# Kernel tuning notes

Measured on AMD Instinct MI355X. Metric: run time of the kernel, lower is better.

The kernel has to match this reference:

```python
import jax, jax.numpy as jnp
import numpy as np

N = 50000   # nodes
E = 800000  # edges (avg degree 16)
IN, H, OUT = 128, 128, 64


def setup_inputs() -> dict:
    key = jax.random.key(0)
    ks = jax.random.split(key, 8)

    def w(k, shape):
        fan_in = shape[0]
        return (jax.random.normal(k, shape, jnp.float32) / np.float32(np.sqrt(fan_in)))

    x = jax.random.normal(ks[0], (N, IN), jnp.float32)
    edge_index = jax.random.randint(ks[1], (2, E), 0, N, jnp.int64)
    return {
        "x": x,
        "edge_index": edge_index,
        "W1": w(ks[2], (IN, H)), "b1": jnp.zeros((H,), jnp.float32),
        "W2": w(ks[3], (H, H)),  "b2": jnp.zeros((H,), jnp.float32),
        "W3": w(ks[4], (H, H)),  "b3": jnp.zeros((H,), jnp.float32),
        "Wd1": w(ks[5], (H, H)), "bd1": jnp.zeros((H,), jnp.float32),
        "Wd2": w(ks[6], (H, OUT)), "bd2": jnp.zeros((OUT,), jnp.float32),
    }


def _gcn_conv(x, src, dst, norm, W, b):
    # x: [N, Cin] -> linear transform, gather along edges, normalized scatter-add
    h = x @ W                                   # [N, Cout]
    msg = h[src] * norm[:, None]                # [E+N, Cout]
    out = jax.ops.segment_sum(msg, dst, num_segments=N)
    return out + b


def reference(x, edge_index, W1, b1, W2, b2, W3, b3, Wd1, bd1, Wd2, bd2):
    # Add self-loops (PyG GCNConv default) and compute symmetric normalization.
    loops = jnp.arange(N, dtype=edge_index.dtype)
    src = jnp.concatenate([edge_index[0], loops])   # [E+N]
    dst = jnp.concatenate([edge_index[1], loops])   # [E+N]
    deg = jax.ops.segment_sum(jnp.ones_like(dst, dtype=x.dtype), dst, num_segments=N)
    dinv = jnp.where(deg > 0, jax.lax.rsqrt(deg), jnp.zeros_like(deg))
    norm = dinv[src] * dinv[dst]                    # [E+N]

    h = jax.nn.relu(_gcn_conv(x, src, dst, norm, W1, b1))
    h = jax.nn.relu(_gcn_conv(h, src, dst, norm, W2, b2))
    h = jax.nn.relu(_gcn_conv(h, src, dst, norm, W3, b3))

    h = jax.nn.relu(h @ Wd1 + bd1)
    return jax.nn.sigmoid(h @ Wd2 + bd2)            # [N, OUT]
```

## Files before the change

kernel.cpp:

```cpp
#include <hip/hip_runtime.h>
#include <hip/hip_bf16.h>
#include <hip/hip_fp16.h>

#define N_NODES 50000
#define N_EDGES 800000
#define C_H 128
#define C_OUT 64
#define NBLK 196
#define TSTRIDE 136
#define E_PAD 950272
#define MM_BLKS 782

typedef __attribute__((ext_vector_type(8))) short bf16x8;
typedef __attribute__((ext_vector_type(4))) float f32x4;

static __device__ __forceinline__ float bf_lo(unsigned int u) { return __uint_as_float(u << 16); }
static __device__ __forceinline__ float bf_hi(unsigned int u) { return __uint_as_float(u & 0xffff0000u); }
static __device__ __forceinline__ unsigned short f2bf(float f) {
    __hip_bfloat16 h = __float2bfloat16(f);
    return *(unsigned short*)&h;
}
static __device__ __forceinline__ unsigned int pack2(float a, float b) {
    return (unsigned int)f2bf(a) | ((unsigned int)f2bf(b) << 16);
}
static __device__ __forceinline__ unsigned short f2h_bits(float f) {
    union { __half h; unsigned short u; } c; c.h = __float2half_rn(f); return c.u;
}
static __device__ __forceinline__ float h_bits2f(unsigned short u) {
    union { __half h; unsigned short u; } c; c.u = u; return __half2float(c.h);
}

__global__ void prep_kernel(const int* __restrict__ dst, int* __restrict__ counts,
                            int* __restrict__ rank,
                            const float* __restrict__ W1, const float* __restrict__ W2,
                            const float* __restrict__ W3, const float* __restrict__ Wd1,
                            const float* __restrict__ Wd2,
                            unsigned short* __restrict__ P1, unsigned short* __restrict__ P2,
                            unsigned short* __restrict__ P3, unsigned short* __restrict__ Pd1,
                            unsigned short* __restrict__ Pd2,
                            unsigned int* __restrict__ epay) {
    int b = blockIdx.x;
    if (b < 3125) {
        int e = b * 256 + threadIdx.x;
        rank[e] = atomicAdd(&counts[dst[e]], 1);
    } else if (b < 3413) {
        int idx = (b - 3125) * 256 + threadIdx.x;
        if (idx < 4 * 16384) {
            int which = idx >> 14;
            int r = idx & 16383;
            const float* W = (which == 0) ? W1 : (which == 1) ? W2 : (which == 2) ? W3 : Wd1;
            unsigned short* P = (which == 0) ? P1 : (which == 1) ? P2 : (which == 2) ? P3 : Pd1;
            int j = r & 7, lane = (r >> 3) & 63, t = r >> 9;
            int nb = t & 7, kb = t >> 3;
            int k = kb * 32 + ((lane >> 4) << 3) + j;
            int n = nb * 16 + (lane & 15);
            P[r] = f2bf(W[(size_t)k * 128 + n]);
        } else {
            int r = idx - 65536;
            if (r < 8192) {
                int j = r & 7, lane = (r >> 3) & 63, t = r >> 9;
                int nb = t & 3, kb = t >> 2;
                int k = kb * 32 + ((lane >> 4) << 3) + j;
                int n = nb * 16 + (lane & 15);
                Pd2[r] = f2bf(Wd2[(size_t)k * 64 + n]);
            }
        }
    } else {
        int i = (b - 3413) * 256 + threadIdx.x;
        *(uint4*)(epay + (size_t)i * 4) = make_uint4(0, 0, 0, 0);
    }
}

__global__ void __launch_bounds__(256) scan1_kernel(const int* __restrict__ counts,
                                                    int* __restrict__ eblk,
                                                    int* __restrict__ bsum,
                                                    float* __restrict__ dinv) {
    __shared__ int ws[4];
    int i = blockIdx.x * 256 + threadIdx.x;
    int v = (i < N_NODES) ? counts[i] : 0;
    if (i < N_NODES) dinv[i] = rsqrtf((float)v + 1.0f);
    int vp = (v + 3) & ~3;
    int lane = threadIdx.x & 63, w = threadIdx.x >> 6;
    int x = vp;
    #pragma unroll
    for (int off = 1; off < 64; off <<= 1) {
        int t = __shfl_up(x, off, 64);
        if (lane >= off) x += t;
    }
    if (lane == 63) ws[w] = x;
    __syncthreads();
    if (threadIdx.x == 0) {
        int run = 0;
        #pragma unroll
        for (int k = 0; k < 4; ++k) { int t = ws[k]; ws[k] = run; run += t; }
        bsum[blockIdx.x] = run;
    }
    __syncthreads();
    if (i < N_NODES) eblk[i] = x - vp + ws[w];
}

__global__ void __launch_bounds__(256) scan2_kernel(const int* __restrict__ bsum,
                                                    int* __restrict__ bo,
                                                    int* __restrict__ rowptr) {
    __shared__ int ws[4];
    int i = threadIdx.x;
    int v = (i < NBLK) ? bsum[i] : 0;
    int lane = i & 63, w = i >> 6;
    int x = v;
    #pragma unroll
    for (int off = 1; off < 64; off <<= 1) {
        int t = __shfl_up(x, off, 64);
        if (lane >= off) x += t;
    }
    if (lane == 63) ws[w] = x;
    __syncthreads();
    if (i == 0) {
        int run = 0;
        #pragma unroll
        for (int k = 0; k < 4; ++k) { int t = ws[k]; ws[k] = run; run += t; }
    }
    __syncthreads();
    int excl = x - v + ws[w];
    if (i < NBLK) bo[i] = excl;
    if (i == 255) rowptr[N_NODES] = excl + v;
}

__global__ void scan3_kernel(const int* __restrict__ eblk, const int* __restrict__ bo,
                             int* __restrict__ rowptr) {
    int i = blockIdx.x * 256 + threadIdx.x;
    if (i < N_NODES) rowptr[i] = eblk[i] + bo[blockIdx.x];
}

__global__ void __launch_bounds__(256) fill_mm_kernel(
        const float* __restrict__ x, const unsigned short* __restrict__ P1,
        unsigned short* __restrict__ XW1,
        const int* __restrict__ src, const int* __restrict__ dst,
        const float* __restrict__ dinv,
        const int* __restrict__ rowptr, const int* __restrict__ rank,
        unsigned int* __restrict__ epay) {
    int b = blockIdx.x;
    if (b < MM_BLKS) {
        const int lane = threadIdx.x & 63;
        const int wave = threadIdx.x >> 6;
        const int wid  = b * 4 + wave;
        if (wid * 16 >= N_NODES) return;
        const int node = wid * 16 + (lane & 15);
        const int quad = lane >> 4;
        f32x4 acc[8];
        #pragma unroll
        for (int nb = 0; nb < 8; ++nb) acc[nb] = (f32x4){0.f, 0.f, 0.f, 0.f};
        #pragma unroll
        for (int kb = 0; kb < 4; ++kb) {
            const float* p = x + (size_t)node * 128 + kb * 32 + quad * 8;
            float4 lo = *(const float4*)p;
            float4 hi = *(const float4*)(p + 4);
            union { bf16x8 v; unsigned int u[4]; } tmp;
            tmp.u[0] = pack2(lo.x, lo.y); tmp.u[1] = pack2(lo.z, lo.w);
            tmp.u[2] = pack2(hi.x, hi.y); tmp.u[3] = pack2(hi.z, hi.w);
            #pragma unroll
            for (int nb = 0; nb < 8; ++nb) {
                bf16x8 wf = *(const bf16x8*)(P1 + ((size_t)(kb * 8 + nb) * 64 + lane) * 8);
                acc[nb] = __builtin_amdgcn_mfma_f32_16x16x32_bf16(wf, tmp.v, acc[nb], 0, 0, 0);
            }
        }
        #pragma unroll
        for (int nb = 0; nb < 8; ++nb) {
            int ch = nb * 16 + quad * 4;
            uint2 o;
            o.x = pack2(acc[nb][0], acc[nb][1]);
            o.y = pack2(acc[nb][2], acc[nb][3]);
            *(uint2*)(XW1 + (size_t)node * C_H + ch) = o;
        }
    } else {
        int e = (b - MM_BLKS) * 256 + threadIdx.x;
        if (e < N_EDGES) {
            int d = dst[e], s = src[e];
            int pos = rowptr[d] + rank[e];
            float nrm = dinv[s] * dinv[d];
            epay[pos] = (unsigned int)s | ((unsigned int)f2h_bits(nrm) << 16);
        }
    }
}

struct Acc8 { float a0, a1, a2, a3, a4, a5, a6, a7; };

static __device__ __forceinline__ unsigned int ev_comp(const uint4 ea, const uint4 eb, int j) {
    switch (j) {
        case 0: return ea.x; case 1: return ea.y; case 2: return ea.z; case 3: return ea.w;
        case 4: return eb.x; case 5: return eb.y; case 6: return eb.z; default: return eb.w;
    }
}
static __device__ __forceinline__ unsigned int ev_comp4(const uint4 ev, int j) {
    switch (j) { case 0: return ev.x; case 1: return ev.y; case 2: return ev.z; default: return ev.w; }
}

#define ROW_FMA(rv, nm) \
    r.a0 = fmaf(bf_lo((rv).x), nm, r.a0); r.a1 = fmaf(bf_hi((rv).x), nm, r.a1); \
    r.a2 = fmaf(bf_lo((rv).y), nm, r.a2); r.a3 = fmaf(bf_hi((rv).y), nm, r.a3); \
    r.a4 = fmaf(bf_lo((rv).z), nm, r.a4); r.a5 = fmaf(bf_hi((rv).z), nm, r.a5); \
    r.a6 = fmaf(bf_lo((rv).w), nm, r.a6); r.a7 = fmaf(bf_hi((rv).w), nm, r.a7);

static __device__ __forceinline__ Acc8 agg_row(
        const int* __restrict__ rowptr,
        const unsigned int* __restrict__ epay,
        const unsigned short* __restrict__ hin,
        const float* __restrict__ dinv,
        int node, int c8) {
    const unsigned short* hc = hin + c8;
    float di = dinv[node], dii = di * di;
    uint4 raw = *(const uint4*)(hc + (size_t)node * C_H);
    Acc8 r;
    r.a0 = bf_lo(raw.x) * dii; r.a1 = bf_hi(raw.x) * dii;
    r.a2 = bf_lo(raw.y) * dii; r.a3 = bf_hi(raw.y) * dii;
    r.a4 = bf_lo(raw.z) * dii; r.a5 = bf_hi(raw.z) * dii;
    r.a6 = bf_lo(raw.w) * dii; r.a7 = bf_hi(raw.w) * dii;

    int beg = rowptr[node], end = rowptr[node + 1];
    int deg = end - beg;
    int n8 = deg >> 3;
    int tail = (deg >> 2) & 1;
    const unsigned int* ep = epay + beg;

    if (n8 > 0) {
        uint4 e0a = *(const uint4*)(ep);
        uint4 e0b = *(const uint4*)(ep + 4);
        uint4 r0[8];
        #pragma unroll
        for (int j = 0; j < 8; ++j)
            r0[j] = *(const uint4*)(hc + (size_t)(ev_comp(e0a, e0b, j) & 0xffffu) * C_H);
        uint4 e1a, e1b;
        if (n8 > 1) {
            e1a = *(const uint4*)(ep + 8);
            e1b = *(const uint4*)(ep + 12);
        }
        for (int k = 0; k + 2 < n8; ++k) {
            uint4 r1[8];
            #pragma unroll
            for (int j = 0; j < 8; ++j)
                r1[j] = *(const uint4*)(hc + (size_t)(ev_comp(e1a, e1b, j) & 0xffffu) * C_H);
            uint4 e2a = *(const uint4*)(ep + ((k + 2) << 3));
            uint4 e2b = *(const uint4*)(ep + ((k + 2) << 3) + 4);
            #pragma unroll
            for (int j = 0; j < 8; ++j) {
                float nm = h_bits2f((unsigned short)(ev_comp(e0a, e0b, j) >> 16));
                ROW_FMA(r0[j], nm);
            }
            e0a = e1a; e0b = e1b; e1a = e2a; e1b = e2b;
            #pragma unroll
            for (int j = 0; j < 8; ++j) r0[j] = r1[j];
        }
        if (n8 > 1) {
            uint4 r1[8];
            #pragma unroll
            for (int j = 0; j < 8; ++j)
                r1[j] = *(const uint4*)(hc + (size_t)(ev_comp(e1a, e1b, j) & 0xffffu) * C_H);
            #pragma unroll
            for (int j = 0; j < 8; ++j) {
                float nm = h_bits2f((unsigned short)(ev_comp(e0a, e0b, j) >> 16));
                ROW_FMA(r0[j], nm);
            }
            #pragma unroll
            for (int j = 0; j < 8; ++j) {
                float nm = h_bits2f((unsigned short)(ev_comp(e1a, e1b, j) >> 16));
                ROW_FMA(r1[j], nm);
            }
        } else {
            #pragma unroll
            for (int j = 0; j < 8; ++j) {
                float nm = h_bits2f((unsigned short)(ev_comp(e0a, e0b, j) >> 16));
                ROW_FMA(r0[j], nm);
            }
        }
    }
    if (tail) {
        uint4 ev = *(const uint4*)(ep + (n8 << 3));
        uint4 rv[4];
        #pragma unroll
        for (int j = 0; j < 4; ++j)
            rv[j] = *(const uint4*)(hc + (size_t)(ev_comp4(ev, j) & 0xffffu) * C_H);
        #pragma unroll
        for (int j = 0; j < 4; ++j) {
            float nm = h_bits2f((unsigned short)(ev_comp4(ev, j) >> 16));
            ROW_FMA(rv[j], nm);
        }
    }
    return r;
}

__global__ void __launch_bounds__(256) gather1_kernel(
        const int* __restrict__ rowptr,
        const unsigned int* __restrict__ epay,
        const float* __restrict__ dinv,
        const unsigned short* __restrict__ hin,
        const float* __restrict__ bias,
        unsigned short* __restrict__ out) {
    int t    = blockIdx.x * 256 + threadIdx.x;
    int node = t >> 4;
    int c8   = (t & 15) << 3;

    Acc8 r = agg_row(rowptr, epay, hin, dinv, node, c8);

    float4 ba = *(const float4*)(bias + c8);
    float4 bb = *(const float4*)(bias + c8 + 4);
    float a0 = fmaxf(r.a0 + ba.x, 0.f), a1 = fmaxf(r.a1 + ba.y, 0.f);
    float a2 = fmaxf(r.a2 + ba.z, 0.f), a3 = fmaxf(r.a3 + ba.w, 0.f);
    float a4 = fmaxf(r.a4 + bb.x, 0.f), a5 = fmaxf(r.a5 + bb.y, 0.f);
    float a6 = fmaxf(r.a6 + bb.z, 0.f), a7 = fmaxf(r.a7 + bb.w, 0.f);
    uint4 o;
    o.x = pack2(a0, a1); o.y = pack2(a2, a3);
    o.z = pack2(a4, a5); o.w = pack2(a6, a7);
    *(uint4*)(out + (size_t)node * C_H + c8) = o;
}

template <bool FINAL>
__global__ void __launch_bounds__(256) fused_layer_kernel(
        const int* __restrict__ rowptr,
        const unsigned int* __restrict__ epay,
        const float* __restrict__ dinv,
        const unsigned short* __restrict__ hin,
        const unsigned short* __restrict__ Wp,
        const float* __restrict__ bias,
        const unsigned short* __restrict__ Wd1p,
        const float* __restrict__ bd1,
        const unsigned short* __restrict__ Wd2p,
        const float* __restrict__ bd2,
        unsigned short* __restrict__ out_b,
        float* __restrict__ out_f) {
    __shared__ unsigned short sG[16 * TSTRIDE];
    const int t = threadIdx.x;

    {
        int nl = t >> 4, c8 = (t & 15) << 3;
        int node = blockIdx.x * 16 + nl;
        Acc8 r = agg_row(rowptr, epay, hin, dinv, node, c8);
        uint4 o;
        o.x = pack2(r.a0, r.a1); o.y = pack2(r.a2, r.a3);
        o.z = pack2(r.a4, r.a5); o.w = pack2(r.a6, r.a7);
        *(uint4*)(sG + nl * TSTRIDE + c8) = o;
    }
    __syncthreads();

    const int lane = t & 63, wave = t >> 6, quad = lane >> 4, row = lane & 15;
    const int node = blockIdx.x * 16 + row;

    f32x4 acc0 = (f32x4){0.f, 0.f, 0.f, 0.f};
    f32x4 acc1 = (f32x4){0.f, 0.f, 0.f, 0.f};
    const int nb0 = 2 * wave, nb1 = 2 * wave + 1;
    #pragma unroll
    for (int kb = 0; kb < 4; ++kb) {
        bf16x8 hf = *(const bf16x8*)(sG + row * TSTRIDE + kb * 32 + quad * 8);
        bf16x8 wf0 = *(const bf16x8*)(Wp + ((size_t)(kb * 8 + nb0) * 64 + lane) * 8);
        bf16x8 wf1 = *(const bf16x8*)(Wp + ((size_t)(kb * 8 + nb1) * 64 + lane) * 8);
        acc0 = __builtin_amdgcn_mfma_f32_16x16x32_bf16(wf0, hf, acc0, 0, 0, 0);
        acc1 = __builtin_amdgcn_mfma_f32_16x16x32_bf16(wf1, hf, acc1, 0, 0, 0);
    }
    float4 ba0 = *(const float4*)(bias + nb0 * 16 + quad * 4);
    float4 ba1 = *(const float4*)(bias + nb1 * 16 + quad * 4);
    float v00 = fmaxf(acc0[0] + ba0.x, 0.f), v01 = fmaxf(acc0[1] + ba0.y, 0.f);
    float v02 = fmaxf(acc0[2] + ba0.z, 0.f), v03 = fmaxf(acc0[3] + ba0.w, 0.f);
    float v10 = fmaxf(acc1[0] + ba1.x, 0.f), v11 = fmaxf(acc1[1] + ba1.y, 0.f);
    float v12 = fmaxf(acc1[2] + ba1.z, 0.f), v13 = fmaxf(acc1[3] + ba1.w, 0.f);

    if (!FINAL) {
        uint2 o0, o1;
        o0.x = pack2(v00, v01); o0.y = pack2(v02, v03);
        o1.x = pack2(v10, v11); o1.y = pack2(v12, v13);
        *(uint2*)(out_b + (size_t)node * C_H + nb0 * 16 + quad * 4) = o0;
        *(uint2*)(out_b + (size_t)node * C_H + nb1 * 16 + quad * 4) = o1;
        return;
    }

    __syncthreads();
    {
        uint2 o0, o1;
        o0.x = pack2(v00, v01); o0.y = pack2(v02, v03);
        o1.x = pack2(v10, v11); o1.y = pack2(v12, v13);
        *(uint2*)(sG + row * TSTRIDE + nb0 * 16 + quad * 4) = o0;
        *(uint2*)(sG + row * TSTRIDE + nb1 * 16 + quad * 4) = o1;
    }
    __syncthreads();

    acc0 = (f32x4){0.f, 0.f, 0.f, 0.f};
    acc1 = (f32x4){0.f, 0.f, 0.f, 0.f};
    #pragma unroll
    for (int kb = 0; kb < 4; ++kb) {
        bf16x8 hf = *(const bf16x8*)(sG + row * TSTRIDE + kb * 32 + quad * 8);
        bf16x8 wf0 = *(const bf16x8*)(Wd1p + ((size_t)(kb * 8 + nb0) * 64 + lane) * 8);
        bf16x8 wf1 = *(const bf16x8*)(Wd1p + ((size_t)(kb * 8 + nb1) * 64 + lane) * 8);
        acc0 = __builtin_amdgcn_mfma_f32_16x16x32_bf16(wf0, hf, acc0, 0, 0, 0);
        acc1 = __builtin_amdgcn_mfma_f32_16x16x32_bf16(wf1, hf, acc1, 0, 0, 0);
    }
    ba0 = *(const float4*)(bd1 + nb0 * 16 + quad * 4);
    ba1 = *(const float4*)(bd1 + nb1 * 16 + quad * 4);
    v00 = fmaxf(acc0[0] + ba0.x, 0.f); v01 = fmaxf(acc0[1] + ba0.y, 0.f);
    v02 = fmaxf(acc0[2] + ba0.z, 0.f); v03 = fmaxf(acc0[3] + ba0.w, 0.f);
    v10 = fmaxf(acc1[0] + ba1.x, 0.f); v11 = fmaxf(acc1[1] + ba1.y, 0.f);
    v12 = fmaxf(acc1[2] + ba1.z, 0.f); v13 = fmaxf(acc1[3] + ba1.w, 0.f);
    __syncthreads();
    {
        uint2 o0, o1;
        o0.x = pack2(v00, v01); o0.y = pack2(v02, v03);
        o1.x = pack2(v10, v11); o1.y = pack2(v12, v13);
        *(uint2*)(sG + row * TSTRIDE + nb0 * 16 + quad * 4) = o0;
        *(uint2*)(sG + row * TSTRIDE + nb1 * 16 + quad * 4) = o1;
    }
    __syncthreads();

    f32x4 acc = (f32x4){0.f, 0.f, 0.f, 0.f};
    #pragma unroll
    for (int kb = 0; kb < 4; ++kb) {
        bf16x8 hf = *(const bf16x8*)(sG + row * TSTRIDE + kb * 32 + quad * 8);
        bf16x8 wf = *(const bf16x8*)(Wd2p + ((size_t)(kb * 4 + wave) * 64 + lane) * 8);
        acc = __builtin_amdgcn_mfma_f32_16x16x32_bf16(wf, hf, acc, 0, 0, 0);
    }
    int ch = wave * 16 + quad * 4;
    float4 b4 = *(const float4*)(bd2 + ch);
    float4 rr;
    rr.x = 1.f / (1.f + expf(-(acc[0] + b4.x)));
    rr.y = 1.f / (1.f + expf(-(acc[1] + b4.y)));
    rr.z = 1.f / (1.f + expf(-(acc[2] + b4.z)));
    rr.w = 1.f / (1.f + expf(-(acc[3] + b4.w)));
    *(float4*)(out_f + (size_t)node * C_OUT + ch) = rr;
}

extern "C" void kernel_launch(void* const* d_in, const int* in_sizes, int n_in,
                              void* d_out, int out_size, void* d_ws, size_t ws_size,
                              hipStream_t stream) {
    const float* x   = (const float*)d_in[0];
    const int*   ei  = (const int*)d_in[1];
    const float* W1  = (const float*)d_in[2];
    const float* b1  = (const float*)d_in[3];
    const float* W2  = (const float*)d_in[4];
    const float* b2  = (const float*)d_in[5];
    const float* W3  = (const float*)d_in[6];
    const float* b3  = (const float*)d_in[7];
    const float* Wd1 = (const float*)d_in[8];
    const float* bd1 = (const float*)d_in[9];
    const float* Wd2 = (const float*)d_in[10];
    const float* bd2 = (const float*)d_in[11];

    const int* src = ei;
    const int* dst = ei + N_EDGES;

    char* base = (char*)d_ws;
    size_t off = 0;
    auto alloc = [&](size_t bytes) { char* p = base + off; off += (bytes + 255) & ~size_t(255); return p; };
    int*            counts = (int*)alloc(50176 * 4);
    unsigned int*   epay   = (unsigned int*)alloc((size_t)E_PAD * 4);
    int*            rank   = (int*)alloc((size_t)N_EDGES * 4);
    float*          dinv   = (float*)alloc(N_NODES * 4);
    int*            rowptr = (int*)alloc((N_NODES + 1) * 4);
    int*            eblk   = (int*)alloc(N_NODES * 4);
    int*            bsum   = (int*)alloc(256 * 4);
    int*            bo     = (int*)alloc(256 * 4);
    unsigned short* XW1    = (unsigned short*)alloc((size_t)N_NODES * C_H * 2);
    unsigned short* bufA   = (unsigned short*)alloc((size_t)N_NODES * C_H * 2);
    unsigned short* bufB   = (unsigned short*)alloc((size_t)N_NODES * C_H * 2);
    unsigned short* P1     = (unsigned short*)alloc(128 * 128 * 2);
    unsigned short* P2     = (unsigned short*)alloc(128 * 128 * 2);
    unsigned short* P3     = (unsigned short*)alloc(128 * 128 * 2);
    unsigned short* Pd1    = (unsigned short*)alloc(128 * 128 * 2);
    unsigned short* Pd2    = (unsigned short*)alloc(128 * 64 * 2);

    const int T = 256;
    dim3 blk(T);
    dim3 gN((N_NODES + T - 1) / T);
    dim3 gPrep(3125 + 288 + 928);
    dim3 gFillMM(MM_BLKS + 3125);
    dim3 gFused(N_NODES / 16);

    hipMemsetAsync(counts, 0, 50176 * 4, stream);
    prep_kernel<<<gPrep, blk, 0, stream>>>(dst, counts, rank,
                                           W1, W2, W3, Wd1, Wd2,
                                           P1, P2, P3, Pd1, Pd2, epay);
    scan1_kernel<<<gN, blk, 0, stream>>>(counts, eblk, bsum, dinv);
    scan2_kernel<<<1, blk, 0, stream>>>(bsum, bo, rowptr);
    scan3_kernel<<<gN, blk, 0, stream>>>(eblk, bo, rowptr);
    fill_mm_kernel<<<gFillMM, blk, 0, stream>>>(x, P1, XW1, src, dst, dinv,
                                                rowptr, rank, epay);

    gather1_kernel<<<gFused, blk, 0, stream>>>(rowptr, epay, dinv, XW1, b1, bufA);
    fused_layer_kernel<false><<<gFused, blk, 0, stream>>>(
        rowptr, epay, dinv, bufA, P2, b2, nullptr, nullptr, nullptr, nullptr, bufB, nullptr);
    fused_layer_kernel<true><<<gFused, blk, 0, stream>>>(
        rowptr, epay, dinv, bufB, P3, b3, Pd1, bd1, Pd2, bd2, nullptr, (float*)d_out);
}
```

Baseline: 255.6 us.

## Split fused gather+matmul layers, slice aggregation by channel for L2 locality

Aggregation is pulled out of the fused layer kernels into a standalone agg_kernel. Its grid puts 8 channel-slice blocks over the same 128 nodes, so each slice gathers a narrower part of the feature table and may get better cache reuse. The matmul and final MLP become separate kernels that read the aggregated rows. Scan2 and scan3 are merged into one kernel, and the software-pipelined edge loop is simplified to a plain loop. In exchange there are more kernel launches and extra global round-trips of the N×128 intermediates.

```diff
diff --git a/kernel.cpp b/kernel.cpp
--- a/kernel.cpp
+++ b/kernel.cpp
@@ -10,6 +10,7 @@
 #define TSTRIDE 136
 #define E_PAD 950272
 #define MM_BLKS 782
+#define AGG_NG 391
 
 typedef __attribute__((ext_vector_type(8))) short bf16x8;
 typedef __attribute__((ext_vector_type(4))) float f32x4;
@@ -99,10 +100,11 @@
     if (i < N_NODES) eblk[i] = x - vp + ws[w];
 }
 
-__global__ void __launch_bounds__(256) scan2_kernel(const int* __restrict__ bsum,
-                                                    int* __restrict__ bo,
+__global__ void __launch_bounds__(256) scanB_kernel(const int* __restrict__ eblk,
+                                                    const int* __restrict__ bsum,
                                                     int* __restrict__ rowptr) {
     __shared__ int ws[4];
+    __shared__ int sbo;
     int i = threadIdx.x;
     int v = (i < NBLK) ? bsum[i] : 0;
     int lane = i & 63, w = i >> 6;
@@ -121,14 +123,11 @@
     }
     __syncthreads();
     int excl = x - v + ws[w];
-    if (i < NBLK) bo[i] = excl;
-    if (i == 255) rowptr[N_NODES] = excl + v;
-}
-
-__global__ void scan3_kernel(const int* __restrict__ eblk, const int* __restrict__ bo,
-                             int* __restrict__ rowptr) {
-    int i = blockIdx.x * 256 + threadIdx.x;
-    if (i < N_NODES) rowptr[i] = eblk[i] + bo[blockIdx.x];
+    if (i == (int)blockIdx.x) sbo = excl;
+    if (blockIdx.x == 0 && i == NBLK - 1) rowptr[N_NODES] = excl + v;
+    __syncthreads();
+    int g = blockIdx.x * 256 + threadIdx.x;
+    if (g < N_NODES) rowptr[g] = eblk[g] + sbo;
 }
 
 __global__ void __launch_bounds__(256) fill_mm_kernel(
@@ -221,55 +220,17 @@
     int tail = (deg >> 2) & 1;
     const unsigned int* ep = epay + beg;
 
-    if (n8 > 0) {
-        uint4 e0a = *(const uint4*)(ep);
-        uint4 e0b = *(const uint4*)(ep + 4);
-        uint4 r0[8];
+    for (int k = 0; k < n8; ++k) {
+        uint4 ea = *(const uint4*)(ep + (k << 3));
+        uint4 eb = *(const uint4*)(ep + (k << 3) + 4);
+        uint4 rv[8];
         #pragma unroll
         for (int j = 0; j < 8; ++j)
-            r0[j] = *(const uint4*)(hc + (size_t)(ev_comp(e0a, e0b, j) & 0xffffu) * C_H);
-        uint4 e1a, e1b;
-        if (n8 > 1) {
-            e1a = *(const uint4*)(ep + 8);
-            e1b = *(const uint4*)(ep + 12);
-        }
-        for (int k = 0; k + 2 < n8; ++k) {
-            uint4 r1[8];
-            #pragma unroll
-            for (int j = 0; j < 8; ++j)
-                r1[j] = *(const uint4*)(hc + (size_t)(ev_comp(e1a, e1b, j) & 0xffffu) * C_H);
-            uint4 e2a = *(const uint4*)(ep + ((k + 2) << 3));
-            uint4 e2b = *(const uint4*)(ep + ((k + 2) << 3) + 4);
-            #pragma unroll
-            for (int j = 0; j < 8; ++j) {
-                float nm = h_bits2f((unsigned short)(ev_comp(e0a, e0b, j) >> 16));
-                ROW_FMA(r0[j], nm);
-            }
-            e0a = e1a; e0b = e1b; e1a = e2a; e1b = e2b;
-            #pragma unroll
-            for (int j = 0; j < 8; ++j) r0[j] = r1[j];
-        }
-        if (n8 > 1) {
-            uint4 r1[8];
-            #pragma unroll
-            for (int j = 0; j < 8; ++j)
-                r1[j] = *(const uint4*)(hc + (size_t)(ev_comp(e1a, e1b, j) & 0xffffu) * C_H);
-            #pragma unroll
-            for (int j = 0; j < 8; ++j) {
-                float nm = h_bits2f((unsigned short)(ev_comp(e0a, e0b, j) >> 16));
-                ROW_FMA(r0[j], nm);
-            }
-            #pragma unroll
-            for (int j = 0; j < 8; ++j) {
-                float nm = h_bits2f((unsigned short)(ev_comp(e1a, e1b, j) >> 16));
-                ROW_FMA(r1[j], nm);
-            }
-        } else {
-            #pragma unroll
-            for (int j = 0; j < 8; ++j) {
-                float nm = h_bits2f((unsigned short)(ev_comp(e0a, e0b, j) >> 16));
-                ROW_FMA(r0[j], nm);
-            }
+            rv[j] = *(const uint4*)(hc + (size_t)(ev_comp(ea, eb, j) & 0xffffu) * C_H);
+        #pragma unroll
+        for (int j = 0; j < 8; ++j) {
+            float nm = h_bits2f((unsigned short)(ev_comp(ea, eb, j) >> 16));
+            ROW_FMA(rv[j], nm);
         }
     }
     if (tail) {
@@ -287,89 +248,110 @@
     return r;
 }
 
-__global__ void __launch_bounds__(256) gather1_kernel(
+template <bool BIASRELU>
+__global__ void __launch_bounds__(256) agg_kernel(
         const int* __restrict__ rowptr,
         const unsigned int* __restrict__ epay,
         const float* __restrict__ dinv,
         const unsigned short* __restrict__ hin,
         const float* __restrict__ bias,
         unsigned short* __restrict__ out) {
-    int t    = blockIdx.x * 256 + threadIdx.x;
-    int node = t >> 4;
-    int c8   = (t & 15) << 3;
+    const int t = threadIdx.x;
+    const unsigned int b = blockIdx.x;
+    const int slice = (int)(b & 7u);
+    const int node  = (int)(b >> 3) * 128 + (t >> 1);
+    if (node >= N_NODES) return;
+    const int c8 = slice * 16 + (t & 1) * 8;
 
     Acc8 r = agg_row(rowptr, epay, hin, dinv, node, c8);
 
-    float4 ba = *(const float4*)(bias + c8);
-    float4 bb = *(const float4*)(bias + c8 + 4);
-    float a0 = fmaxf(r.a0 + ba.x, 0.f), a1 = fmaxf(r.a1 + ba.y, 0.f);
-    float a2 = fmaxf(r.a2 + ba.z, 0.f), a3 = fmaxf(r.a3 + ba.w, 0.f);
-    float a4 = fmaxf(r.a4 + bb.x, 0.f), a5 = fmaxf(r.a5 + bb.y, 0.f);
-    float a6 = fmaxf(r.a6 + bb.z, 0.f), a7 = fmaxf(r.a7 + bb.w, 0.f);
+    float a0, a1, a2, a3, a4, a5, a6, a7;
+    if (BIASRELU) {
+        float4 ba = *(const float4*)(bias + c8);
+        float4 bb = *(const float4*)(bias + c8 + 4);
+        a0 = fmaxf(r.a0 + ba.x, 0.f); a1 = fmaxf(r.a1 + ba.y, 0.f);
+        a2 = fmaxf(r.a2 + ba.z, 0.f); a3 = fmaxf(r.a3 + ba.w, 0.f);
+        a4 = fmaxf(r.a4 + bb.x, 0.f); a5 = fmaxf(r.a5 + bb.y, 0.f);
+        a6 = fmaxf(r.a6 + bb.z, 0.f); a7 = fmaxf(r.a7 + bb.w, 0.f);
+    } else {
+        a0 = r.a0; a1 = r.a1; a2 = r.a2; a3 = r.a3;
+        a4 = r.a4; a5 = r.a5; a6 = r.a6; a7 = r.a7;
+    }
     uint4 o;
     o.x = pack2(a0, a1); o.y = pack2(a2, a3);
     o.z = pack2(a4, a5); o.w = pack2(a6, a7);
     *(uint4*)(out + (size_t)node * C_H + c8) = o;
 }
 
-template <bool FINAL>
-__global__ void __launch_bounds__(256) fused_layer_kernel(
-        const int* __restrict__ rowptr,
-        const unsigned int* __restrict__ epay,
-        const float* __restrict__ dinv,
+__global__ void __launch_bounds__(256) mmbr_kernel(
         const unsigned short* __restrict__ hin,
         const unsigned short* __restrict__ Wp,
         const float* __restrict__ bias,
-        const unsigned short* __restrict__ Wd1p,
-        const float* __restrict__ bd1,
-        const unsigned short* __restrict__ Wd2p,
-        const float* __restrict__ bd2,
-        unsigned short* __restrict__ out_b,
+        unsigned short* __restrict__ out) {
+    const int lane = threadIdx.x & 63;
+    const int wave = threadIdx.x >> 6;
+    const int wid  = blockIdx.x * 4 + wave;
+    if (wid * 16 >= N_NODES) return;
+    const int node = wid * 16 + (lane & 15);
+    const int quad = lane >> 4;
+    f32x4 acc[8];
+    #pragma unroll
+    for (int nb = 0; nb < 8; ++nb) acc[nb] = (f32x4){0.f, 0.f, 0.f, 0.f};
+    #pragma unroll
+    for (int kb = 0; kb < 4; ++kb) {
+        bf16x8 hf = *(const bf16x8*)(hin + (size_t)node * C_H + kb * 32 + quad * 8);
+        #pragma unroll
+        for (int nb = 0; nb < 8; ++nb) {
+            bf16x8 wf = *(const bf16x8*)(Wp + ((size_t)(kb * 8 + nb) * 64 + lane) * 8);
+            acc[nb] = __builtin_amdgcn_mfma_f32_16x16x32_bf16(wf, hf, acc[nb], 0, 0, 0);
+        }
+    }
+    #pragma unroll
+    for (int nb = 0; nb < 8; ++nb) {
+        int ch = nb * 16 + quad * 4;
+        float4 bb = *(const float4*)(bias + ch);
+        uint2 o;
+        o.x = pack2(fmaxf(acc[nb][0] + bb.x, 0.f), fmaxf(acc[nb][1] + bb.y, 0.f));
+        o.y = pack2(fmaxf(acc[nb][2] + bb.z, 0.f), fmaxf(acc[nb][3] + bb.w, 0.f));
+        *(uint2*)(out + (size_t)node * C_H + ch) = o;
+    }
+}
+
+__global__ void __launch_bounds__(256) final_kernel(
+        const unsigned short* __restrict__ g3,
+        const unsigned short* __restrict__ P3p, const float* __restrict__ b3,
+        const unsigned short* __restrict__ Wd1p, const float* __restrict__ bd1,
+        const unsigned short* __restrict__ Wd2p, const float* __restrict__ bd2,
         float* __restrict__ out_f) {
     __shared__ unsigned short sG[16 * TSTRIDE];
     const int t = threadIdx.x;
-
     {
         int nl = t >> 4, c8 = (t & 15) << 3;
         int node = blockIdx.x * 16 + nl;
-        Acc8 r = agg_row(rowptr, epay, hin, dinv, node, c8);
-        uint4 o;
-        o.x = pack2(r.a0, r.a1); o.y = pack2(r.a2, r.a3);
-        o.z = pack2(r.a4, r.a5); o.w = pack2(r.a6, r.a7);
-        *(uint4*)(sG + nl * TSTRIDE + c8) = o;
+        *(uint4*)(sG + nl * TSTRIDE + c8) = *(const uint4*)(g3 + (size_t)node * C_H + c8);
     }
     __syncthreads();
 
     const int lane = t & 63, wave = t >> 6, quad = lane >> 4, row = lane & 15;
     const int node = blockIdx.x * 16 + row;
+    const int nb0 = 2 * wave, nb1 = 2 * wave + 1;
 
     f32x4 acc0 = (f32x4){0.f, 0.f, 0.f, 0.f};
     f32x4 acc1 = (f32x4){0.f, 0.f, 0.f, 0.f};
-    const int nb0 = 2 * wave, nb1 = 2 * wave + 1;
     #pragma unroll
     for (int kb = 0; kb < 4; ++kb) {
         bf16x8 hf = *(const bf16x8*)(sG + row * TSTRIDE + kb * 32 + quad * 8);
-        bf16x8 wf0 = *(const bf16x8*)(Wp + ((size_t)(kb * 8 + nb0) * 64 + lane) * 8);
-        bf16x8 wf1 = *(const bf16x8*)(Wp + ((size_t)(kb * 8 + nb1) * 64 + lane) * 8);
+        bf16x8 wf0 = *(const bf16x8*)(P3p + ((size_t)(kb * 8 + nb0) * 64 + lane) * 8);
+        bf16x8 wf1 = *(const bf16x8*)(P3p + ((size_t)(kb * 8 + nb1) * 64 + lane) * 8);
         acc0 = __builtin_amdgcn_mfma_f32_16x16x32_bf16(wf0, hf, acc0, 0, 0, 0);
         acc1 = __builtin_amdgcn_mfma_f32_16x16x32_bf16(wf1, hf, acc1, 0, 0, 0);
     }
-    float4 ba0 = *(const float4*)(bias + nb0 * 16 + quad * 4);
-    float4 ba1 = *(const float4*)(bias + nb1 * 16 + quad * 4);
+    float4 ba0 = *(const float4*)(b3 + nb0 * 16 + quad * 4);
+    float4 ba1 = *(const float4*)(b3 + nb1 * 16 + quad * 4);
     float v00 = fmaxf(acc0[0] + ba0.x, 0.f), v01 = fmaxf(acc0[1] + ba0.y, 0.f);
     float v02 = fmaxf(acc0[2] + ba0.z, 0.f), v03 = fmaxf(acc0[3] + ba0.w, 0.f);
     float v10 = fmaxf(acc1[0] + ba1.x, 0.f), v11 = fmaxf(acc1[1] + ba1.y, 0.f);
     float v12 = fmaxf(acc1[2] + ba1.z, 0.f), v13 = fmaxf(acc1[3] + ba1.w, 0.f);
-
-    if (!FINAL) {
-        uint2 o0, o1;
-        o0.x = pack2(v00, v01); o0.y = pack2(v02, v03);
-        o1.x = pack2(v10, v11); o1.y = pack2(v12, v13);
-        *(uint2*)(out_b + (size_t)node * C_H + nb0 * 16 + quad * 4) = o0;
-        *(uint2*)(out_b + (size_t)node * C_H + nb1 * 16 + quad * 4) = o1;
-        return;
-    }
-
     __syncthreads();
     {
         uint2 o0, o1;
@@ -452,7 +434,6 @@
     int*            rowptr = (int*)alloc((N_NODES + 1) * 4);
     int*            eblk   = (int*)alloc(N_NODES * 4);
     int*            bsum   = (int*)alloc(256 * 4);
-    int*            bo     = (int*)alloc(256 * 4);
     unsigned short* XW1    = (unsigned short*)alloc((size_t)N_NODES * C_H * 2);
     unsigned short* bufA   = (unsigned short*)alloc((size_t)N_NODES * C_H * 2);
     unsigned short* bufB   = (unsigned short*)alloc((size_t)N_NODES * C_H * 2);
@@ -467,21 +448,23 @@
     dim3 gN((N_NODES + T - 1) / T);
     dim3 gPrep(3125 + 288 + 928);
     dim3 gFillMM(MM_BLKS + 3125);
-    dim3 gFused(N_NODES / 16);
+    dim3 gAgg(AGG_NG * 8);
+    dim3 gMM(MM_BLKS);
+    dim3 gFinal(N_NODES / 16);
 
     hipMemsetAsync(counts, 0, 50176 * 4, stream);
     prep_kernel<<<gPrep, blk, 0, stream>>>(dst, counts, rank,
                                            W1, W2, W3, Wd1, Wd2,
                                            P1, P2, P3, Pd1, Pd2, epay);
     scan1_kernel<<<gN, blk, 0, stream>>>(counts, eblk, bsum, dinv);
-    scan2_kernel<<<1, blk, 0, stream>>>(bsum, bo, rowptr);
-    scan3_kernel<<<gN, blk, 0, stream>>>(eblk, bo, rowptr);
+    scanB_kernel<<<gN, blk, 0, stream>>>(eblk, bsum, rowptr);
     fill_mm_kernel<<<gFillMM, blk, 0, stream>>>(x, P1, XW1, src, dst, dinv,
                                                 rowptr, rank, epay);
 
-    gather1_kernel<<<gFused, blk, 0, stream>>>(rowptr, epay, dinv, XW1, b1, bufA);
-    fused_layer_kernel<false><<<gFused, blk, 0, stream>>>(
-        rowptr, epay, dinv, bufA, P2, b2, nullptr, nullptr, nullptr, nullptr, bufB, nullptr);
-    fused_layer_kernel<true><<<gFused, blk, 0, stream>>>(
-        rowptr, epay, dinv, bufB, P3, b3, Pd1, bd1, Pd2, bd2, nullptr, (float*)d_out);
-}
+    agg_kernel<true><<<gAgg, blk, 0, stream>>>(rowptr, epay, dinv, XW1, b1, bufA);
+    agg_kernel<false><<<gAgg, blk, 0, stream>>>(rowptr, epay, dinv, bufA, nullptr, bufB);
+    mmbr_kernel<<<gMM, blk, 0, stream>>>(bufB, P2, b2, XW1);
+    agg_kernel<false><<<gAgg, blk, 0, stream>>>(rowptr, epay, dinv, XW1, nullptr, bufB);
+    final_kernel<<<gFinal, blk, 0, stream>>>(bufB, P3, b3, Pd1, bd1, Pd2, bd2,
+                                             (float*)d_out);
+}
```

Measured after the change: 404.9 us. +58.4%, slower.
